# Optimization experiments

Hardware: AMD Instinct MI355X
Metric: run time of the kernel (lower is better)

The kernel has to match this reference:

```python
import jax, jax.numpy as jnp
import numpy as np
from jax import lax

SCALE = 2
KSIZE = 5
RGB_RANGE = 255.0
RGB_MEAN = (0.4488, 0.4371, 0.404)


def setup_inputs() -> dict:
    key = jax.random.key(0)
    ks = jax.random.split(key, 8)
    N, C, H, W = 4, 3, 128, 128
    G0 = 64
    s = SCALE
    x = jax.random.normal(ks[0], (N, C, H, W), dtype=jnp.float32)
    # relative position matrix: (1, (H*s)*(W*s), 3), values in [0,1)
    pos_mat = jax.random.uniform(ks[1], (1, H * s * W * s, 3), dtype=jnp.float32)
    conv_w = jax.random.normal(ks[2], (G0, C, KSIZE, KSIZE), dtype=jnp.float32) * 0.05
    conv_b = jax.random.normal(ks[3], (G0,), dtype=jnp.float32) * 0.05
    w1 = jax.random.normal(ks[4], (3, 256), dtype=jnp.float32) * 0.05
    b1 = jax.random.normal(ks[5], (256,), dtype=jnp.float32) * 0.05
    w2 = jax.random.normal(ks[6], (256, 9 * G0 * 3), dtype=jnp.float32) * 0.05
    b2 = jax.random.normal(ks[7], (9 * G0 * 3,), dtype=jnp.float32) * 0.05
    return {"x": x, "pos_mat": pos_mat, "conv_w": conv_w, "conv_b": conv_b,
            "w1": w1, "b1": b1, "w2": w2, "b2": b2}


def _unfold3(feat):
    # torch F.unfold(feat, 3, padding=1) ordering: channel-major then (ki, kj)
    N, C, H, W = feat.shape
    p = jnp.pad(feat, ((0, 0), (0, 0), (1, 1), (1, 1)))
    patches = jnp.stack([p[:, :, i:i + H, j:j + W]
                         for i in range(3) for j in range(3)], axis=2)  # [N,C,9,H,W]
    return patches.reshape(N, C * 9, H * W)  # [N, C*9, L]


def reference(x, pos_mat, conv_w, conv_b, w1, b1, w2, b2):
    s = SCALE
    N, _, H, W = x.shape
    # Feature extraction: conv5x5 (SAME) + ReLU
    feat = lax.conv_general_dilated(x, conv_w, (1, 1), 'SAME',
                                    dimension_numbers=('NCHW', 'OIHW', 'NCHW'))
    feat = jax.nn.relu(feat + conv_b[None, :, None, None])  # [N, G0, H, W]
    G0 = feat.shape[1]
    K = G0 * 9
    # Pos2Weight MLP: per output-pixel dynamic conv weights
    p = pos_mat.reshape(-1, 3)  # [(H*s)*(W*s), 3]
    lw = jax.nn.relu(p @ w1 + b1) @ w2 + b2  # [(H*s)*(W*s), K*3]
    # reshape to [s^2, H*W, K, 3] matching torch permute pipeline
    lw = lw.reshape(H, s, W, s, K, 3).transpose(1, 3, 0, 2, 4, 5).reshape(s * s, H * W, K, 3)
    # unfold 3x3 patches (repeat_x just tiles identical copies; compute once)
    cols = _unfold3(feat).transpose(0, 2, 1)  # [N, L, K], L = H*W
    # per-pixel matmul: out[n,p,l,c] = sum_k cols[n,l,k] * lw[p,l,k,c]
    out = jnp.einsum('nlk,plkc->nplc', cols, lw)  # [N, s^2, L, 3]
    # pixel-shuffle style rearrangement to [N, 3, H*s, W*s]
    out = out.reshape(N, s, s, H, W, 3).transpose(0, 5, 3, 1, 4, 2)
    out = out.reshape(N, 3, H * s, W * s)
    # add_mean (MeanShift sign=+1, std=1)
    mean = jnp.asarray(RGB_MEAN, dtype=out.dtype) * RGB_RANGE
    return out + mean[None, :, None, None]
```

## Files before the change

kernel.cpp:

```cpp
#include <hip/hip_runtime.h>

#define HW   128
#define OHW  256
#define G0n  64
#define HID  256
#define NOUT 1728
#define NB   4

typedef __attribute__((ext_vector_type(8))) short bf16x8;
typedef __attribute__((ext_vector_type(4))) float f32x4;
typedef __attribute__((ext_vector_type(4))) unsigned int u32x4;
typedef __attribute__((ext_vector_type(2))) unsigned int u32x2;

__device__ __forceinline__ unsigned short f2bf(float f) {
    unsigned int u = __builtin_bit_cast(unsigned int, f);
    u += 0x7fffu + ((u >> 16) & 1u);
    return (unsigned short)(u >> 16);
}
__device__ __forceinline__ float bflo(unsigned int d) {
    return __builtin_bit_cast(float, d << 16);
}
__device__ __forceinline__ float bfhi(unsigned int d) {
    return __builtin_bit_cast(float, d & 0xffff0000u);
}

__device__ __forceinline__ void barrier_ldsonly() {
    __builtin_amdgcn_sched_barrier(0);
    asm volatile("s_waitcnt lgkmcnt(0)" ::: "memory");
    __builtin_amdgcn_s_barrier();
    __builtin_amdgcn_sched_barrier(0);
}

__global__ __launch_bounds__(256) void prep_w2t(const float* __restrict__ w2,
                                                unsigned short* __restrict__ w2t) {
    __shared__ float t[64][65];
    int kb = blockIdx.x & 3, cb = blockIdx.x >> 2;
    int lc = threadIdx.x & 63, lr = threadIdx.x >> 6;
    #pragma unroll
    for (int i = 0; i < 16; ++i) {
        int kk = lr + i * 4;
        t[kk][lc] = w2[(kb * 64 + kk) * NOUT + cb * 64 + lc];
    }
    __syncthreads();
    #pragma unroll
    for (int i = 0; i < 16; ++i) {
        int cc = lr + i * 4;
        w2t[(cb * 64 + cc) * 256 + kb * 64 + lc] = f2bf(t[lc][cc]);
    }
}

__global__ __launch_bounds__(256) void conv5_relu_kernel(
    const float* __restrict__ x, const float* __restrict__ cw,
    const float* __restrict__ cb, float* __restrict__ feat)
{
    int idx = blockIdx.x * 256 + threadIdx.x;
    int w4 = (idx & 31) * 4;
    int h  = (idx >> 5) & 127;
    int g  = (idx >> 12) & 63;
    int n  = idx >> 18;
    float bv = cb[g];
    float a[4] = {bv, bv, bv, bv};
    const float* wp = cw + g * 75;
    #pragma unroll
    for (int ci = 0; ci < 3; ++ci) {
        const float* xr = x + (n * 3 + ci) * (HW * HW);
        #pragma unroll
        for (int ki = 0; ki < 5; ++ki) {
            int hh = h + ki - 2;
            if (hh < 0 || hh >= HW) continue;
            const float* row = xr + hh * HW;
            float f[8];
            if (w4 != 0 && w4 != 124) {
                float2 u0 = *(const float2*)(row + w4 - 2);
                float2 u1 = *(const float2*)(row + w4);
                float2 u2 = *(const float2*)(row + w4 + 2);
                float2 u3 = *(const float2*)(row + w4 + 4);
                f[0] = u0.x; f[1] = u0.y; f[2] = u1.x; f[3] = u1.y;
                f[4] = u2.x; f[5] = u2.y; f[6] = u3.x; f[7] = u3.y;
            } else {
                #pragma unroll
                for (int j = 0; j < 8; ++j) {
                    int ww = w4 - 2 + j;
                    f[j] = (ww >= 0 && ww < HW) ? row[ww] : 0.0f;
                }
            }
            float wt[5];
            #pragma unroll
            for (int kj = 0; kj < 5; ++kj) wt[kj] = wp[ci * 25 + ki * 5 + kj];
            #pragma unroll
            for (int j = 0; j < 4; ++j)
                #pragma unroll
                for (int kj = 0; kj < 5; ++kj)
                    a[j] = fmaf(f[j + kj], wt[kj], a[j]);
        }
    }
    float4 o;
    o.x = fmaxf(a[0], 0.f); o.y = fmaxf(a[1], 0.f);
    o.z = fmaxf(a[2], 0.f); o.w = fmaxf(a[3], 0.f);
    *(float4*)&feat[((n * G0n + g) * HW + h) * HW + w4] = o;
}

__global__ __launch_bounds__(256) void gemm_lw(
    const unsigned short* __restrict__ w2t, const float* __restrict__ pos,
    const float* __restrict__ w1, const float* __restrict__ b1,
    const float* __restrict__ b2, unsigned short* __restrict__ lw)
{
    __shared__ __align__(16) unsigned short AL[64 * 260];

    const int tid = threadIdx.x;
    const int bx = blockIdx.x & 31, by = blockIdx.x >> 5;
    const int oy0 = by * 8, ox0 = bx * 8;

    {
        int px = tid >> 2, q = tid & 3;
        int rr = (oy0 + (px >> 3)) * OHW + (ox0 + (px & 7));
        float p0 = pos[rr * 3 + 0], p1 = pos[rr * 3 + 1], p2 = pos[rr * 3 + 2];
        #pragma unroll
        for (int j = 0; j < 16; ++j) {
            int k0 = q * 4 + j * 16;
            float4 wa = *(const float4*)&w1[k0];
            float4 wb = *(const float4*)&w1[HID + k0];
            float4 wc = *(const float4*)&w1[2 * HID + k0];
            float4 bb = *(const float4*)&b1[k0];
            unsigned short h0s = f2bf(fmaxf(fmaf(p0, wa.x, fmaf(p1, wb.x, fmaf(p2, wc.x, bb.x))), 0.f));
            unsigned short h1s = f2bf(fmaxf(fmaf(p0, wa.y, fmaf(p1, wb.y, fmaf(p2, wc.y, bb.y))), 0.f));
            unsigned short h2s = f2bf(fmaxf(fmaf(p0, wa.z, fmaf(p1, wb.z, fmaf(p2, wc.z, bb.z))), 0.f));
            unsigned short h3s = f2bf(fmaxf(fmaf(p0, wa.w, fmaf(p1, wb.w, fmaf(p2, wc.w, bb.w))), 0.f));
            u32x2 pk;
            pk.x = (unsigned)h0s | ((unsigned)h1s << 16);
            pk.y = (unsigned)h2s | ((unsigned)h3s << 16);
            *(u32x2*)&AL[px * 260 + k0] = pk;
        }
    }
    __syncthreads();

    const int lane = tid & 63, nq = tid >> 6;
    const int cl = lane & 15, hi = lane >> 4;
    bf16x8 afrag[4][8];
    #pragma unroll
    for (int m = 0; m < 4; ++m)
        #pragma unroll
        for (int k8 = 0; k8 < 8; ++k8)
            afrag[m][k8] = *(const bf16x8*)&AL[(m * 16 + cl) * 260 + k8 * 32 + hi * 8];
    __syncthreads();

    const size_t rowbase = (size_t)blockIdx.x * 64;
    const int srow = tid >> 2, sq = tid & 3;

    for (int ch = 0; ch < 9; ++ch) {
        f32x4 acc[4][3];
        #pragma unroll
        for (int m = 0; m < 4; ++m)
            #pragma unroll
            for (int j = 0; j < 3; ++j)
                acc[m][j] = (f32x4){0.f, 0.f, 0.f, 0.f};
        #pragma unroll
        for (int ks = 0; ks < 8; ++ks) {
            bf16x8 bfrag[3];
            #pragma unroll
            for (int j = 0; j < 3; ++j) {
                int col = ch * 192 + nq * 48 + j * 16 + cl;
                bfrag[j] = *(const bf16x8*)&w2t[(size_t)col * 256 + ks * 32 + hi * 8];
            }
            #pragma unroll
            for (int m = 0; m < 4; ++m)
                #pragma unroll
                for (int j = 0; j < 3; ++j)
                    acc[m][j] = __builtin_amdgcn_mfma_f32_16x16x32_bf16(
                        afrag[m][ks], bfrag[j], acc[m][j], 0, 0, 0);
        }
        barrier_ldsonly();
        #pragma unroll
        for (int j = 0; j < 3; ++j) {
            int lcol = nq * 48 + j * 16 + cl;
            float bv = b2[ch * 192 + lcol];
            #pragma unroll
            for (int m = 0; m < 4; ++m)
                #pragma unroll
                for (int r = 0; r < 4; ++r)
                    AL[(m * 16 + hi * 4 + r) * 200 + lcol] = f2bf(acc[m][j][r] + bv);
        }
        barrier_ldsonly();
        unsigned short* dst = lw + (rowbase + srow) * NOUT + ch * 192;
        #pragma unroll
        for (int s = 0; s < 6; ++s) {
            int off = (sq + s * 4) * 8;
            *(u32x4*)(dst + off) = *(const u32x4*)&AL[srow * 200 + off];
        }
    }
}

__global__ __launch_bounds__(256) void einsum_out(
    const float* __restrict__ feat, const unsigned short* __restrict__ lw,
    float* __restrict__ out)
{
    __shared__ __align__(8) unsigned short FT[64 * 6 * 4 * 6];

    const int tid = threadIdx.x;
    const int bx = blockIdx.x & 31, by = blockIdx.x >> 5;
    const int oy0 = by * 8, ox0 = bx * 8;
    const int h0 = by * 4,  w0 = bx * 4;

    for (int i = tid; i < 64 * 6 * 4 * 6; i += 256) {
        int c = i % 6;
        int t = i / 6;
        int n = t & 3;
        t >>= 2;
        int r  = t % 6;
        int ci = t / 6;
        int gh = h0 - 1 + r, gw = w0 - 1 + c;
        float v = 0.0f;
        if (gh >= 0 && gh < HW && gw >= 0 && gw < HW)
            v = feat[((n * G0n + ci) * HW + gh) * HW + gw];
        FT[i] = f2bf(v);
    }
    __syncthreads();

    const int px = tid >> 2, n = tid & 3;
    const int iy = (px >> 3) >> 1;
    const int ix = (px & 7) >> 1;
    const bool podd = (ix & 1) != 0;
    const int ixa = ix & ~1;

    const u32x4* lwp = (const u32x4*)(lw + ((size_t)blockIdx.x * 64 + px) * NOUT);
    float o0 = 0.f, o1 = 0.f, o2 = 0.f;

    for (int g = 0; g < 8; ++g) {
        u32x4 LA[14], LB[14];
        #pragma unroll
        for (int t = 0; t < 14; ++t) LA[t] = lwp[g * 27 + t];
        #pragma unroll
        for (int t = 0; t < 14; ++t) LB[t] = (t + 13 < 27) ? lwp[g * 27 + 13 + t] : (u32x4){0,0,0,0};

        #pragma unroll
        for (int cl8 = 0; cl8 < 8; ++cl8) {
            int ci = g * 8 + cl8;
            float fv[9];
            #pragma unroll
            for (int di = 0; di < 3; ++di) {
                int rb = ((ci * 6 + iy + di) * 4 + n) * 6 + ixa;
                unsigned u0 = *(const unsigned*)&FT[rb];
                unsigned u1 = *(const unsigned*)&FT[rb + 2];
                fv[di * 3 + 0] = podd ? bfhi(u0) : bflo(u0);
                fv[di * 3 + 1] = podd ? bflo(u1) : bfhi(u0);
                fv[di * 3 + 2] = podd ? bfhi(u1) : bflo(u1);
            }
            #pragma unroll
            for (int ktl = 0; ktl < 9; ++ktl) {
                #pragma unroll
                for (int c = 0; c < 3; ++c) {
                    int idx = cl8 * 27 + ktl * 3 + c;
                    unsigned d;
                    if (idx < 108) d = LA[idx >> 3][(idx >> 1) & 3];
                    else { int i2 = idx - 104; d = LB[i2 >> 3][(i2 >> 1) & 3]; }
                    float v = (idx & 1) ? bfhi(d) : bflo(d);
                    if (c == 0) o0 = fmaf(fv[ktl], v, o0);
                    else if (c == 1) o1 = fmaf(fv[ktl], v, o1);
                    else o2 = fmaf(fv[ktl], v, o2);
                }
            }
        }
    }

    int oy = oy0 + (px >> 3), ox = ox0 + (px & 7);
    out[((n * 3 + 0) * OHW + oy) * OHW + ox] = o0 + 0.4488f * 255.0f;
    out[((n * 3 + 1) * OHW + oy) * OHW + ox] = o1 + 0.4371f * 255.0f;
    out[((n * 3 + 2) * OHW + oy) * OHW + ox] = o2 + 0.4040f * 255.0f;
}

extern "C" void kernel_launch(void* const* d_in, const int* in_sizes, int n_in,
                              void* d_out, int out_size, void* d_ws, size_t ws_size,
                              hipStream_t stream) {
    (void)in_sizes; (void)n_in; (void)out_size; (void)ws_size;
    const float* x      = (const float*)d_in[0];
    const float* posm   = (const float*)d_in[1];
    const float* conv_w = (const float*)d_in[2];
    const float* conv_b = (const float*)d_in[3];
    const float* w1     = (const float*)d_in[4];
    const float* b1     = (const float*)d_in[5];
    const float* w2     = (const float*)d_in[6];
    const float* b2     = (const float*)d_in[7];
    float* out = (float*)d_out;

    unsigned short* w2t = (unsigned short*)d_ws;
    float* feat = (float*)((char*)d_ws + 884736);
    const size_t lw_off = 884736u + 16777216u;
    unsigned short* lwbuf = (unsigned short*)((char*)d_ws + lw_off);

    prep_w2t<<<108, 256, 0, stream>>>(w2, w2t);
    conv5_relu_kernel<<<(NB * G0n * HW * 32) / 256, 256, 0, stream>>>(x, conv_w, conv_b, feat);
    gemm_lw<<<1024, 256, 0, stream>>>(w2t, posm, w1, b1, b2, lwbuf);
    einsum_out<<<1024, 256, 0, stream>>>(feat, lwbuf, out);
}
```

Baseline: 239.5 us.

## Double gemm_lw row tile with pipelined fragments; stage lw through LDS in einsum

gemm_lw now processes 128 rows per block (512 blocks) with separate A and C staging buffers. A and B fragments are software-pipelined from LDS and global memory instead of holding all A fragments in registers, which doubles reuse of each loaded w2t fragment. einsum_out stages each 192-column chunk of lw into LDS with padding to 4 elements per tap, so each thread reads its weights as 8-byte LDS loads instead of holding 28 u32x4 registers. This adds more barriers per chunk and larger LDS footprints that limit occupancy.

```diff
diff --git a/kernel.cpp b/kernel.cpp
--- a/kernel.cpp
+++ b/kernel.cpp
@@ -100,24 +100,27 @@
     *(float4*)&feat[((n * G0n + g) * HW + h) * HW + w4] = o;
 }
 
-__global__ __launch_bounds__(256) void gemm_lw(
+__global__ __launch_bounds__(256, 1) void gemm_lw(
     const unsigned short* __restrict__ w2t, const float* __restrict__ pos,
     const float* __restrict__ w1, const float* __restrict__ b1,
     const float* __restrict__ b2, unsigned short* __restrict__ lw)
 {
-    __shared__ __align__(16) unsigned short AL[64 * 260];
+    __shared__ __align__(16) unsigned short A[128 * 260];
+    __shared__ __align__(16) unsigned short CS[128 * 200];
 
     const int tid = threadIdx.x;
-    const int bx = blockIdx.x & 31, by = blockIdx.x >> 5;
-    const int oy0 = by * 8, ox0 = bx * 8;
+    const int b = blockIdx.x;
 
     {
-        int px = tid >> 2, q = tid & 3;
-        int rr = (oy0 + (px >> 3)) * OHW + (ox0 + (px & 7));
+        int px2 = tid >> 1, q = tid & 1;
+        int cb = 2 * b + (px2 >> 6);
+        int px64 = px2 & 63;
+        int bx = cb & 31, by = cb >> 5;
+        int rr = (by * 8 + (px64 >> 3)) * OHW + (bx * 8 + (px64 & 7));
         float p0 = pos[rr * 3 + 0], p1 = pos[rr * 3 + 1], p2 = pos[rr * 3 + 2];
         #pragma unroll
-        for (int j = 0; j < 16; ++j) {
-            int k0 = q * 4 + j * 16;
+        for (int j = 0; j < 32; ++j) {
+            int k0 = q * 128 + j * 4;
             float4 wa = *(const float4*)&w1[k0];
             float4 wb = *(const float4*)&w1[HID + k0];
             float4 wc = *(const float4*)&w1[2 * HID + k0];
@@ -129,63 +132,76 @@
             u32x2 pk;
             pk.x = (unsigned)h0s | ((unsigned)h1s << 16);
             pk.y = (unsigned)h2s | ((unsigned)h3s << 16);
-            *(u32x2*)&AL[px * 260 + k0] = pk;
+            *(u32x2*)&A[px2 * 260 + k0] = pk;
         }
     }
     __syncthreads();
 
     const int lane = tid & 63, nq = tid >> 6;
     const int cl = lane & 15, hi = lane >> 4;
-    bf16x8 afrag[4][8];
-    #pragma unroll
-    for (int m = 0; m < 4; ++m)
-        #pragma unroll
-        for (int k8 = 0; k8 < 8; ++k8)
-            afrag[m][k8] = *(const bf16x8*)&AL[(m * 16 + cl) * 260 + k8 * 32 + hi * 8];
-    __syncthreads();
-
-    const size_t rowbase = (size_t)blockIdx.x * 64;
+    const size_t rowbase = (size_t)b * 128;
     const int srow = tid >> 2, sq = tid & 3;
 
     for (int ch = 0; ch < 9; ++ch) {
-        f32x4 acc[4][3];
-        #pragma unroll
-        for (int m = 0; m < 4; ++m)
+        f32x4 acc[8][3];
+        #pragma unroll
+        for (int m = 0; m < 8; ++m)
             #pragma unroll
             for (int j = 0; j < 3; ++j)
                 acc[m][j] = (f32x4){0.f, 0.f, 0.f, 0.f};
+
+        const unsigned short* wp = w2t + ((size_t)(ch * 192 + nq * 48 + cl)) * 256 + hi * 8;
+        bf16x8 bfr[3][3];
+        #pragma unroll
+        for (int j = 0; j < 3; ++j) bfr[0][j] = *(const bf16x8*)(wp + j * 4096);
+        #pragma unroll
+        for (int j = 0; j < 3; ++j) bfr[1][j] = *(const bf16x8*)(wp + j * 4096 + 32);
+        bf16x8 afr[2][8];
+        #pragma unroll
+        for (int m = 0; m < 8; ++m)
+            afr[0][m] = *(const bf16x8*)&A[(m * 16 + cl) * 260 + hi * 8];
+
         #pragma unroll
         for (int ks = 0; ks < 8; ++ks) {
-            bf16x8 bfrag[3];
-            #pragma unroll
-            for (int j = 0; j < 3; ++j) {
-                int col = ch * 192 + nq * 48 + j * 16 + cl;
-                bfrag[j] = *(const bf16x8*)&w2t[(size_t)col * 256 + ks * 32 + hi * 8];
-            }
-            #pragma unroll
-            for (int m = 0; m < 4; ++m)
+            if (ks < 7) {
+                #pragma unroll
+                for (int m = 0; m < 8; ++m)
+                    afr[(ks + 1) & 1][m] =
+                        *(const bf16x8*)&A[(m * 16 + cl) * 260 + (ks + 1) * 32 + hi * 8];
+            }
+            if (ks < 6) {
+                #pragma unroll
+                for (int j = 0; j < 3; ++j)
+                    bfr[(ks + 2) % 3][j] = *(const bf16x8*)(wp + j * 4096 + (ks + 2) * 32);
+            }
+            #pragma unroll
+            for (int m = 0; m < 8; ++m)
                 #pragma unroll
                 for (int j = 0; j < 3; ++j)
                     acc[m][j] = __builtin_amdgcn_mfma_f32_16x16x32_bf16(
-                        afrag[m][ks], bfrag[j], acc[m][j], 0, 0, 0);
-        }
+                        afr[ks & 1][m], bfr[ks % 3][j], acc[m][j], 0, 0, 0);
+        }
+
         barrier_ldsonly();
         #pragma unroll
         for (int j = 0; j < 3; ++j) {
             int lcol = nq * 48 + j * 16 + cl;
             float bv = b2[ch * 192 + lcol];
             #pragma unroll
-            for (int m = 0; m < 4; ++m)
+            for (int m = 0; m < 8; ++m)
                 #pragma unroll
                 for (int r = 0; r < 4; ++r)
-                    AL[(m * 16 + hi * 4 + r) * 200 + lcol] = f2bf(acc[m][j][r] + bv);
+                    CS[(m * 16 + hi * 4 + r) * 200 + lcol] = f2bf(acc[m][j][r] + bv);
         }
         barrier_ldsonly();
-        unsigned short* dst = lw + (rowbase + srow) * NOUT + ch * 192;
-        #pragma unroll
-        for (int s = 0; s < 6; ++s) {
-            int off = (sq + s * 4) * 8;
-            *(u32x4*)(dst + off) = *(const u32x4*)&AL[srow * 200 + off];
+        #pragma unroll
+        for (int r2 = 0; r2 < 128; r2 += 64) {
+            unsigned short* dst = lw + (rowbase + srow + r2) * NOUT + ch * 192;
+            #pragma unroll
+            for (int s = 0; s < 6; ++s) {
+                int off = (sq + s * 4) * 8;
+                *(u32x4*)(dst + off) = *(const u32x4*)&CS[(srow + r2) * 200 + off];
+            }
         }
     }
 }
@@ -195,6 +211,7 @@
     float* __restrict__ out)
 {
     __shared__ __align__(8) unsigned short FT[64 * 6 * 4 * 6];
+    __shared__ __align__(16) unsigned short LW[64 * 260];
 
     const int tid = threadIdx.x;
     const int bx = blockIdx.x & 31, by = blockIdx.x >> 5;
@@ -214,58 +231,79 @@
             v = feat[((n * G0n + ci) * HW + gh) * HW + gw];
         FT[i] = f2bf(v);
     }
-    __syncthreads();
-
-    const int px = tid >> 2, n = tid & 3;
-    const int iy = (px >> 3) >> 1;
-    const int ix = (px & 7) >> 1;
+
+    const int row = tid >> 2, q = tid & 3;
+    const int epx = tid >> 2, en = tid & 3;
+    const int iy = (epx >> 3) >> 1;
+    const int ix = (epx & 7) >> 1;
     const bool podd = (ix & 1) != 0;
     const int ixa = ix & ~1;
-
-    const u32x4* lwp = (const u32x4*)(lw + ((size_t)blockIdx.x * 64 + px) * NOUT);
     float o0 = 0.f, o1 = 0.f, o2 = 0.f;
 
-    for (int g = 0; g < 8; ++g) {
-        u32x4 LA[14], LB[14];
-        #pragma unroll
-        for (int t = 0; t < 14; ++t) LA[t] = lwp[g * 27 + t];
-        #pragma unroll
-        for (int t = 0; t < 14; ++t) LB[t] = (t + 13 < 27) ? lwp[g * 27 + 13 + t] : (u32x4){0,0,0,0};
-
-        #pragma unroll
-        for (int cl8 = 0; cl8 < 8; ++cl8) {
-            int ci = g * 8 + cl8;
-            float fv[9];
-            #pragma unroll
-            for (int di = 0; di < 3; ++di) {
-                int rb = ((ci * 6 + iy + di) * 4 + n) * 6 + ixa;
-                unsigned u0 = *(const unsigned*)&FT[rb];
-                unsigned u1 = *(const unsigned*)&FT[rb + 2];
-                fv[di * 3 + 0] = podd ? bfhi(u0) : bflo(u0);
-                fv[di * 3 + 1] = podd ? bflo(u1) : bfhi(u0);
-                fv[di * 3 + 2] = podd ? bfhi(u1) : bflo(u1);
-            }
-            #pragma unroll
-            for (int ktl = 0; ktl < 9; ++ktl) {
-                #pragma unroll
-                for (int c = 0; c < 3; ++c) {
-                    int idx = cl8 * 27 + ktl * 3 + c;
-                    unsigned d;
-                    if (idx < 108) d = LA[idx >> 3][(idx >> 1) & 3];
-                    else { int i2 = idx - 104; d = LB[i2 >> 3][(i2 >> 1) & 3]; }
-                    float v = (idx & 1) ? bfhi(d) : bflo(d);
-                    if (c == 0) o0 = fmaf(fv[ktl], v, o0);
-                    else if (c == 1) o1 = fmaf(fv[ktl], v, o1);
-                    else o2 = fmaf(fv[ktl], v, o2);
+    for (int ch = 0; ch < 9; ++ch) {
+        __syncthreads();
+        {
+            const unsigned short* src =
+                lw + ((size_t)blockIdx.x * 64 + row) * NOUT + ch * 192 + q * 48;
+            u32x4 in4[6];
+            #pragma unroll
+            for (int t = 0; t < 6; ++t) in4[t] = *(const u32x4*)(src + t * 8);
+            const unsigned* in = (const unsigned*)in4;
+            unsigned short* dstl = LW + row * 260 + q * 64;
+            #pragma unroll
+            for (int l = 0; l < 16; ++l) {
+                int s = 3 * l;
+                unsigned lo, hi2;
+                if ((s & 1) == 0) {
+                    lo  = in[s >> 1];
+                    hi2 = in[(s >> 1) + 1];
+                } else {
+                    lo  = (in[s >> 1] >> 16) | (in[(s >> 1) + 1] << 16);
+                    hi2 = in[(s >> 1) + 1] >> 16;
                 }
-            }
-        }
-    }
-
-    int oy = oy0 + (px >> 3), ox = ox0 + (px & 7);
-    out[((n * 3 + 0) * OHW + oy) * OHW + ox] = o0 + 0.4488f * 255.0f;
-    out[((n * 3 + 1) * OHW + oy) * OHW + ox] = o1 + 0.4371f * 255.0f;
-    out[((n * 3 + 2) * OHW + oy) * OHW + ox] = o2 + 0.4040f * 255.0f;
+                u32x2 pk; pk.x = lo; pk.y = hi2;
+                *(u32x2*)(dstl + l * 4) = pk;
+            }
+        }
+        __syncthreads();
+
+        const char* lwp = (const char*)LW + epx * 520;
+        int k0 = ch * 64;
+        int t3a = k0 / 3;
+        int t3b = (k0 + 63) / 3;
+        auto do_t3 = [&](int t3, bool guard) {
+            int ci = t3 / 3;
+            int di = t3 - ci * 3;
+            int rb = ((ci * 6 + iy + di) * 4 + en) * 6 + ixa;
+            unsigned u0 = *(const unsigned*)&FT[rb];
+            unsigned u1 = *(const unsigned*)&FT[rb + 2];
+            float f0 = podd ? bfhi(u0) : bflo(u0);
+            float f1 = podd ? bflo(u1) : bfhi(u0);
+            float f2 = podd ? bfhi(u1) : bflo(u1);
+            int ktb = 3 * t3 - k0;
+            #pragma unroll
+            for (int dj = 0; dj < 3; ++dj) {
+                int kt = ktb + dj;
+                float fvv = dj == 0 ? f0 : (dj == 1 ? f1 : f2);
+                if (guard) {
+                    fvv = ((unsigned)kt < 64u) ? fvv : 0.0f;
+                    kt = kt < 0 ? 0 : (kt > 63 ? 63 : kt);
+                }
+                u32x2 d = *(const u32x2*)(lwp + (unsigned)(kt * 8));
+                o0 = fmaf(fvv, bflo(d.x), o0);
+                o1 = fmaf(fvv, bfhi(d.x), o1);
+                o2 = fmaf(fvv, bflo(d.y), o2);
+            }
+        };
+        do_t3(t3a, true);
+        for (int t3 = t3a + 1; t3 < t3b; ++t3) do_t3(t3, false);
+        do_t3(t3b, true);
+    }
+
+    int oy = oy0 + (epx >> 3), ox = ox0 + (epx & 7);
+    out[((en * 3 + 0) * OHW + oy) * OHW + ox] = o0 + 0.4488f * 255.0f;
+    out[((en * 3 + 1) * OHW + oy) * OHW + ox] = o1 + 0.4371f * 255.0f;
+    out[((en * 3 + 2) * OHW + oy) * OHW + ox] = o2 + 0.4040f * 255.0f;
 }
 
 extern "C" void kernel_launch(void* const* d_in, const int* in_sizes, int n_in,
@@ -289,6 +327,6 @@
 
     prep_w2t<<<108, 256, 0, stream>>>(w2, w2t);
     conv5_relu_kernel<<<(NB * G0n * HW * 32) / 256, 256, 0, stream>>>(x, conv_w, conv_b, feat);
-    gemm_lw<<<1024, 256, 0, stream>>>(w2t, posm, w1, b1, b2, lwbuf);
+    gemm_lw<<<512, 256, 0, stream>>>(w2t, posm, w1, b1, b2, lwbuf);
     einsum_out<<<1024, 256, 0, stream>>>(feat, lwbuf, out);
 }
```

After: 271.5 us. 1.13x slower.
